# Performance work log

Hardware: AMD Instinct MI355X
Metric: run time of the kernel (lower is better)

Reference implementation:

```python
import jax, jax.numpy as jnp
import numpy as np

N_VARS = 2048
N_LAYERS = 8
NODES = 4096
FAN_IN = 4
BATCH = 8192


def setup_inputs() -> dict:
    key = jax.random.key(0)
    k1, k2 = jax.random.split(key)
    x = jax.random.uniform(k1, (BATCH, N_VARS), dtype=jnp.float32)
    marginalized_variables = jnp.zeros((N_VARS,), dtype=bool)
    # child_idx[l, n, f]: index of the f-th child of node n in layer l,
    # pointing into the previous layer's 4096 outputs (leaves for l=0).
    child_idx = jax.random.randint(k2, (N_LAYERS, NODES, FAN_IN), 0, NODES, dtype=jnp.int64)
    return {"x": x, "marginalized_variables": marginalized_variables, "child_idx": child_idx}


def reference(x, marginalized_variables, child_idx):
    # Leaf literals: positive literal = x[:, v], negative literal = 1 - x[:, v].
    # Marginalized variables output 1.0 for both literals.
    leaves = jnp.concatenate([x, 1.0 - x], axis=1)            # [B, 2V]
    marg = jnp.tile(marginalized_variables, 2)                 # [2V]
    cur = jnp.where(marg[None, :], jnp.ones((), dtype=leaves.dtype), leaves)
    n_layers = child_idx.shape[0]
    for l in range(n_layers):  # fixed small layer loop; each layer fully vectorized
        gathered = cur[:, child_idx[l]]                        # [B, NODES, FAN_IN]
        if l % 2 == 0:  # AND layer: product of children
            cur = jnp.prod(gathered, axis=-1)                  # [B, NODES]
        else:            # OR layer: sum of children
            cur = jnp.sum(gathered, axis=-1)                   # [B, NODES]
    # Root OR node over the final layer -> [B, 1]
    return jnp.sum(cur, axis=1, keepdims=True)
```

## Files before the change

### kernel.cpp

```cpp
#include <hip/hip_runtime.h>

constexpr int N_VARS   = 2048;
constexpr int NODES    = 4096;
constexpr int N_LAYERS = 8;
constexpr int BATCH    = 8192;
constexpr int THREADS  = 1024;
constexpr int RPB      = 2;
constexpr int NPT      = NODES / THREADS;

__device__ __forceinline__ float bflo(unsigned w) { return __uint_as_float(w << 16); }
__device__ __forceinline__ float bfhi(unsigned w) { return __uint_as_float(w & 0xffff0000u); }
__device__ __forceinline__ unsigned bfpack(float a, float b) {
  unsigned ua = __float_as_uint(a), ub = __float_as_uint(b);
  ua = (ua + 0x7fffu + ((ua >> 16) & 1u)) >> 16;
  ub = (ub + 0x7fffu + ((ub >> 16) & 1u)) & 0xffff0000u;
  return ua | ub;
}

template <int MODE>
__device__ __forceinline__ ushort4 get_idx(const void* p, int n) {
  if (MODE == 0) return ((const ushort4*)p)[n];
  if (MODE == 1) {
    int4 c = ((const int4*)p)[n];
    return make_ushort4((unsigned short)c.x, (unsigned short)c.y,
                        (unsigned short)c.z, (unsigned short)c.w);
  }
  const int* q = (const int*)p + (size_t)n * 8;
  return make_ushort4((unsigned short)q[0], (unsigned short)q[2],
                      (unsigned short)q[4], (unsigned short)q[6]);
}
template <int MODE> __device__ __forceinline__ size_t layer_bytes() {
  return MODE == 0 ? (size_t)NODES * 8 : MODE == 1 ? (size_t)NODES * 16
                                                   : (size_t)NODES * 32;
}

template <int MODE>
__device__ __forceinline__ void prod_pass(const float2* A, unsigned* B,
                                          const void* idx, int t) {
#pragma unroll
  for (int i = 0; i < NPT; ++i) {
    const int n = t + i * THREADS;
    ushort4 c = get_idx<MODE>(idx, n);
    float2 a = A[c.x], b = A[c.y], d = A[c.z], e = A[c.w];
    B[n] = bfpack(a.x * b.x * d.x * e.x, a.y * b.y * d.y * e.y);
  }
}

template <int MODE>
__device__ __forceinline__ void sum_pass(const unsigned* B, float2* A,
                                         const void* idx, int t) {
#pragma unroll
  for (int i = 0; i < NPT; ++i) {
    const int n = t + i * THREADS;
    ushort4 c = get_idx<MODE>(idx, n);
    unsigned a = B[c.x], b = B[c.y], d = B[c.z], e = B[c.w];
    A[n] = make_float2(bflo(a) + bflo(b) + bflo(d) + bflo(e),
                       bfhi(a) + bfhi(b) + bfhi(d) + bfhi(e));
  }
}

template <int MODE>
__device__ __forceinline__ void spn_body(const float* __restrict__ x,
                                         const unsigned char* __restrict__ marg,
                                         const void* __restrict__ idx,
                                         float* __restrict__ out,
                                         float2* A,
                                         unsigned* B) {
  const int t = threadIdx.x;
  const int row0 = blockIdx.x * RPB;
  const float* x0 = x + (size_t)row0 * N_VARS;
  const float* x1 = x0 + N_VARS;

#pragma unroll
  for (int i = 0; i < N_VARS / THREADS; ++i) {
    const int j = t + i * THREADS;
    const float a = x0[j], b = x1[j];
    const bool m = marg[j] != 0;
    A[j]          = make_float2(m ? 1.f : a,       m ? 1.f : b);
    A[N_VARS + j] = make_float2(m ? 1.f : 1.f - a, m ? 1.f : 1.f - b);
  }

  const char* ib = (const char*)idx;
  const size_t LB = layer_bytes<MODE>();
  __syncthreads();
  prod_pass<MODE>(A, B, ib + 0 * LB, t); __syncthreads();
  sum_pass <MODE>(B, A, ib + 1 * LB, t); __syncthreads();
  prod_pass<MODE>(A, B, ib + 2 * LB, t); __syncthreads();
  sum_pass <MODE>(B, A, ib + 3 * LB, t); __syncthreads();
  prod_pass<MODE>(A, B, ib + 4 * LB, t); __syncthreads();
  sum_pass <MODE>(B, A, ib + 5 * LB, t); __syncthreads();
  prod_pass<MODE>(A, B, ib + 6 * LB, t); __syncthreads();

  float s0 = 0.f, s1 = 0.f;
  {
    const void* L7 = ib + 7 * LB;
#pragma unroll
    for (int i = 0; i < NPT; ++i) {
      const int n = t + i * THREADS;
      ushort4 c = get_idx<MODE>(L7, n);
      unsigned a = B[c.x], b = B[c.y], d = B[c.z], e = B[c.w];
      s0 += bflo(a) + bflo(b) + bflo(d) + bflo(e);
      s1 += bfhi(a) + bfhi(b) + bfhi(d) + bfhi(e);
    }
  }
#pragma unroll
  for (int off = 32; off > 0; off >>= 1) {
    s0 += __shfl_down(s0, off);
    s1 += __shfl_down(s1, off);
  }
  if ((t & 63) == 0) A[t >> 6] = make_float2(s0, s1);
  __syncthreads();
  if (t == 0) {
    float2 tot = A[0];
#pragma unroll
    for (int w = 1; w < THREADS / 64; ++w) { tot.x += A[w].x; tot.y += A[w].y; }
    ((float2*)out)[blockIdx.x] = tot;
  }
}

__global__ __launch_bounds__(THREADS, 8) void spn_packed(
    const float* __restrict__ x, const unsigned char* __restrict__ marg,
    const ushort4* __restrict__ idx, float* __restrict__ out) {
  __shared__ float2   A[NODES];
  __shared__ unsigned B[NODES];
  spn_body<0>(x, marg, idx, out, A, B);
}

__global__ __launch_bounds__(THREADS, 8) void spn_raw(
    const float* __restrict__ x, const unsigned char* __restrict__ marg,
    const int* __restrict__ cidx, float* __restrict__ out) {
  __shared__ float2   A[NODES];
  __shared__ unsigned B[NODES];
  int acc = 0;
#pragma unroll
  for (int k = 0; k < 8; ++k) acc |= cidx[2 * k + 1];
  if (acc == 0) spn_body<2>(x, marg, cidx, out, A, B);
  else          spn_body<1>(x, marg, cidx, out, A, B);
}

__global__ __launch_bounds__(64) void prep_idx(const int* __restrict__ cidx,
                                               ushort4* __restrict__ out) {
  const int gid  = blockIdx.x;
  const int l    = gid >> 6;
  const int cgrp = gid & 63;
  const int lane = threadIdx.x;
  const size_t n = (size_t)l * NODES + cgrp * 64 + lane;

  int acc = 0;
#pragma unroll
  for (int k = 0; k < 8; ++k) acc |= cidx[2 * k + 1];

  ushort4 r;
  if (acc == 0) {
    const int4* p = (const int4*)cidx + n * 2;
    int4 u = p[0], v = p[1];
    r = make_ushort4((unsigned short)u.x, (unsigned short)u.z,
                     (unsigned short)v.x, (unsigned short)v.z);
  } else {
    int4 u = ((const int4*)cidx)[n];
    r = make_ushort4((unsigned short)u.x, (unsigned short)u.y,
                     (unsigned short)u.z, (unsigned short)u.w);
  }
  const unsigned w0 = (unsigned)r.x | ((unsigned)r.y << 16);
  const unsigned w1 = (unsigned)r.z | ((unsigned)r.w << 16);
  const int mask = ((l & 1) == 0) ? 15 : 31;

  unsigned hcnt = 0;
  ushort4 mine = r;
  for (int k = 0; k < 64; ++k) {
    const unsigned a0 = __shfl(w0, k);
    const unsigned a1 = __shfl(w1, k);
    unsigned short v4[4] = {(unsigned short)(a0 & 0xffffu), (unsigned short)(a0 >> 16),
                            (unsigned short)(a1 & 0xffffu), (unsigned short)(a1 >> 16)};
    int bank[4];
#pragma unroll
    for (int j = 0; j < 4; ++j) bank[j] = v4[j] & mask;
    unsigned cnt[4];
#pragma unroll
    for (int j = 0; j < 4; ++j) cnt[j] = __shfl(hcnt, bank[j]);
    int slot[4]; unsigned used = 0;
    unsigned short o[4];
#pragma unroll
    for (int j = 0; j < 4; ++j) {
      unsigned eff = cnt[j];
#pragma unroll
      for (int p2 = 0; p2 < 4; ++p2)
        if (p2 < j && bank[p2] == bank[j]) eff += 1u << (8 * slot[p2]);
      const unsigned m2 = eff | used;
      int best = 0; unsigned bv = m2 & 0xffu;
#pragma unroll
      for (int s = 1; s < 4; ++s) {
        const unsigned q = (m2 >> (8 * s)) & 0xffu;
        if (q < bv) { bv = q; best = s; }
      }
      slot[j] = best; used |= 0xffu << (8 * best); o[best] = v4[j];
    }
#pragma unroll
    for (int j = 0; j < 4; ++j)
      if (lane == bank[j]) hcnt += 1u << (8 * slot[j]);
    if (lane == k) mine = make_ushort4(o[0], o[1], o[2], o[3]);
  }
  out[n] = mine;
}

extern "C" void kernel_launch(void* const* d_in, const int* in_sizes, int n_in,
                              void* d_out, int out_size, void* d_ws, size_t ws_size,
                              hipStream_t stream) {
  const float* x          = (const float*)d_in[0];
  const unsigned char* mg = (const unsigned char*)d_in[1];
  const int* cidx         = (const int*)d_in[2];
  float* out              = (float*)d_out;

  const size_t need = (size_t)N_LAYERS * NODES * sizeof(ushort4);
  if (ws_size >= need) {
    ushort4* packed = (ushort4*)d_ws;
    hipLaunchKernelGGL(prep_idx, dim3(N_LAYERS * 64), dim3(64), 0, stream,
                       cidx, packed);
    hipLaunchKernelGGL(spn_packed, dim3(BATCH / RPB), dim3(THREADS), 0, stream,
                       x, mg, packed, out);
  } else {
    hipLaunchKernelGGL(spn_raw, dim3(BATCH / RPB), dim3(THREADS), 0, stream,
                       x, mg, cidx, out);
  }
}
```

Baseline: 212.7 us.

## Duplicate float2 node buffer with XOR swizzle to cut LDS bank conflicts

Keeps a second, XOR-8-swizzled copy of the float2 node array in dynamic shared memory and writes both copies in the leaf and sum passes. The index-prep kernel now chooses, per child, whichever copy lands in a less loaded bank and encodes that choice in bit 12 of the packed index. This is meant to reduce bank conflicts in the product-pass gathers. In exchange it adds extra LDS writes, raises shared memory to 80KB per block and halves the block size to 512 threads, which may lower occupancy.

```diff
diff --git a/kernel.cpp b/kernel.cpp
--- a/kernel.cpp
+++ b/kernel.cpp
@@ -4,9 +4,10 @@
 constexpr int NODES    = 4096;
 constexpr int N_LAYERS = 8;
 constexpr int BATCH    = 8192;
-constexpr int THREADS  = 1024;
+constexpr int THREADS  = 512;
 constexpr int RPB      = 2;
 constexpr int NPT      = NODES / THREADS;
+constexpr size_t SMEM  = (size_t)NODES * 2 * 8 + (size_t)NODES * 4;
 
 __device__ __forceinline__ float bflo(unsigned w) { return __uint_as_float(w << 16); }
 __device__ __forceinline__ float bfhi(unsigned w) { return __uint_as_float(w & 0xffff0000u); }
@@ -54,8 +55,10 @@
     const int n = t + i * THREADS;
     ushort4 c = get_idx<MODE>(idx, n);
     unsigned a = B[c.x], b = B[c.y], d = B[c.z], e = B[c.w];
-    A[n] = make_float2(bflo(a) + bflo(b) + bflo(d) + bflo(e),
-                       bfhi(a) + bfhi(b) + bfhi(d) + bfhi(e));
+    float2 v = make_float2(bflo(a) + bflo(b) + bflo(d) + bflo(e),
+                           bfhi(a) + bfhi(b) + bfhi(d) + bfhi(e));
+    A[n]                 = v;
+    A[NODES + (n ^ 8)]   = v;
   }
 }
 
@@ -76,8 +79,12 @@
     const int j = t + i * THREADS;
     const float a = x0[j], b = x1[j];
     const bool m = marg[j] != 0;
-    A[j]          = make_float2(m ? 1.f : a,       m ? 1.f : b);
-    A[N_VARS + j] = make_float2(m ? 1.f : 1.f - a, m ? 1.f : 1.f - b);
+    float2 lo = make_float2(m ? 1.f : a,       m ? 1.f : b);
+    float2 hi = make_float2(m ? 1.f : 1.f - a, m ? 1.f : 1.f - b);
+    A[j]                          = lo;
+    A[NODES + (j ^ 8)]            = lo;
+    A[N_VARS + j]                 = hi;
+    A[NODES + ((N_VARS + j) ^ 8)] = hi;
   }
 
   const char* ib = (const char*)idx;
@@ -118,19 +125,21 @@
   }
 }
 
-__global__ __launch_bounds__(THREADS, 8) void spn_packed(
+extern __shared__ char smem[];
+
+__global__ __launch_bounds__(THREADS) void spn_packed(
     const float* __restrict__ x, const unsigned char* __restrict__ marg,
     const ushort4* __restrict__ idx, float* __restrict__ out) {
-  __shared__ float2   A[NODES];
-  __shared__ unsigned B[NODES];
+  float2*   A = (float2*)smem;
+  unsigned* B = (unsigned*)(smem + NODES * 16);
   spn_body<0>(x, marg, idx, out, A, B);
 }
 
-__global__ __launch_bounds__(THREADS, 8) void spn_raw(
+__global__ __launch_bounds__(THREADS) void spn_raw(
     const float* __restrict__ x, const unsigned char* __restrict__ marg,
     const int* __restrict__ cidx, float* __restrict__ out) {
-  __shared__ float2   A[NODES];
-  __shared__ unsigned B[NODES];
+  float2*   A = (float2*)smem;
+  unsigned* B = (unsigned*)(smem + NODES * 16);
   int acc = 0;
 #pragma unroll
   for (int k = 0; k < 8; ++k) acc |= cidx[2 * k + 1];
@@ -163,7 +172,8 @@
   }
   const unsigned w0 = (unsigned)r.x | ((unsigned)r.y << 16);
   const unsigned w1 = (unsigned)r.z | ((unsigned)r.w << 16);
-  const int mask = ((l & 1) == 0) ? 15 : 31;
+  const bool dual  = ((l & 1) == 0);
+  const int  kmask = dual ? 15 : 31;
 
   unsigned hcnt = 0;
   ushort4 mine = r;
@@ -172,32 +182,52 @@
     const unsigned a1 = __shfl(w1, k);
     unsigned short v4[4] = {(unsigned short)(a0 & 0xffffu), (unsigned short)(a0 >> 16),
                             (unsigned short)(a1 & 0xffffu), (unsigned short)(a1 >> 16)};
-    int bank[4];
-#pragma unroll
-    for (int j = 0; j < 4; ++j) bank[j] = v4[j] & mask;
-    unsigned cnt[4];
-#pragma unroll
-    for (int j = 0; j < 4; ++j) cnt[j] = __shfl(hcnt, bank[j]);
-    int slot[4]; unsigned used = 0;
+    int b0[4], b1[4];
+    unsigned c0[4], c1[4];
+#pragma unroll
+    for (int j = 0; j < 4; ++j) {
+      b0[j] = v4[j] & kmask;
+      b1[j] = dual ? (b0[j] ^ 8) : b0[j];
+    }
+#pragma unroll
+    for (int j = 0; j < 4; ++j) c0[j] = __shfl(hcnt, b0[j]);
+#pragma unroll
+    for (int j = 0; j < 4; ++j) c1[j] = dual ? __shfl(hcnt, b1[j]) : 0u;
+
+    int slot[4], keyj[4];
     unsigned short o[4];
+    unsigned usedmask = 0;
 #pragma unroll
     for (int j = 0; j < 4; ++j) {
-      unsigned eff = cnt[j];
+      unsigned adj0 = 0, adj1 = 0;
 #pragma unroll
       for (int p2 = 0; p2 < 4; ++p2)
-        if (p2 < j && bank[p2] == bank[j]) eff += 1u << (8 * slot[p2]);
-      const unsigned m2 = eff | used;
-      int best = 0; unsigned bv = m2 & 0xffu;
-#pragma unroll
-      for (int s = 1; s < 4; ++s) {
-        const unsigned q = (m2 >> (8 * s)) & 0xffu;
-        if (q < bv) { bv = q; best = s; }
+        if (p2 < j) {
+          if (keyj[p2] == b0[j]) adj0 += 1u << (8 * slot[p2]);
+          if (dual && keyj[p2] == b1[j]) adj1 += 1u << (8 * slot[p2]);
+        }
+      const unsigned e0 = c0[j] + adj0;
+      const unsigned e1 = dual ? (c1[j] + adj1) : 0xffffffffu;
+      int best = 0, bm = 0; unsigned bv = 0x10000u;
+#pragma unroll
+      for (int s = 0; s < 4; ++s) {
+        if ((usedmask >> s) & 1) continue;
+        const unsigned q0 = (e0 >> (8 * s)) & 0xffu;
+        if (q0 < bv) { bv = q0; best = s; bm = 0; }
+        if (dual) {
+          const unsigned q1 = (e1 >> (8 * s)) & 0xffu;
+          if (q1 < bv) { bv = q1; best = s; bm = 1; }
+        }
       }
-      slot[j] = best; used |= 0xffu << (8 * best); o[best] = v4[j];
+      slot[j] = best; usedmask |= 1u << best;
+      keyj[j] = bm ? b1[j] : b0[j];
+      o[best] = dual ? (unsigned short)(((unsigned)bm << 12) |
+                                        ((unsigned)v4[j] ^ ((unsigned)bm << 3)))
+                     : v4[j];
     }
 #pragma unroll
     for (int j = 0; j < 4; ++j)
-      if (lane == bank[j]) hcnt += 1u << (8 * slot[j]);
+      if (lane == keyj[j]) hcnt += 1u << (8 * slot[j]);
     if (lane == k) mine = make_ushort4(o[0], o[1], o[2], o[3]);
   }
   out[n] = mine;
@@ -211,15 +241,20 @@
   const int* cidx         = (const int*)d_in[2];
   float* out              = (float*)d_out;
 
+  (void)hipFuncSetAttribute((const void*)spn_packed,
+                            hipFuncAttributeMaxDynamicSharedMemorySize, (int)SMEM);
+  (void)hipFuncSetAttribute((const void*)spn_raw,
+                            hipFuncAttributeMaxDynamicSharedMemorySize, (int)SMEM);
+
   const size_t need = (size_t)N_LAYERS * NODES * sizeof(ushort4);
   if (ws_size >= need) {
     ushort4* packed = (ushort4*)d_ws;
     hipLaunchKernelGGL(prep_idx, dim3(N_LAYERS * 64), dim3(64), 0, stream,
                        cidx, packed);
-    hipLaunchKernelGGL(spn_packed, dim3(BATCH / RPB), dim3(THREADS), 0, stream,
+    hipLaunchKernelGGL(spn_packed, dim3(BATCH / RPB), dim3(THREADS), SMEM, stream,
                        x, mg, packed, out);
   } else {
-    hipLaunchKernelGGL(spn_raw, dim3(BATCH / RPB), dim3(THREADS), 0, stream,
+    hipLaunchKernelGGL(spn_raw, dim3(BATCH / RPB), dim3(THREADS), SMEM, stream,
                        x, mg, cidx, out);
   }
 }
```

Measured after the change: 275.1 us. +29.3%, slower.
